# Kernel tuning notes

Hardware: AMD Instinct MI355X
Metric: run time of the kernel (lower is better)

## Reference

```python
import jax, jax.numpy as jnp
import numpy as np

LE_LAMBDA = 0.01  # le_lambda from __init__
V, D = 100000, 128
B, C, NEG, P = 16384, 10, 50, 2000


def setup_inputs() -> dict:
    key = jax.random.key(0)
    k1, k2, k3, k4, k5, k6 = jax.random.split(key, 6)
    return {
        "input_labels": jax.random.randint(k1, (B,), 0, V),
        "pos_labels": jax.random.randint(k2, (B, C), 0, V),
        "neg_labels": jax.random.randint(k3, (B, NEG), 0, V),
        "pairs": jax.random.randint(k4, (P, 2), 0, V),
        "in_embed": jax.random.normal(k5, (V, D), dtype=jnp.float32),
        "out_embed": jax.random.normal(k6, (V, D), dtype=jnp.float32),
    }


def reference(input_labels, pos_labels, neg_labels, pairs, in_embed, out_embed):
    # --- skip-gram negative-sampling loss ---
    ie = in_embed[input_labels]          # [B, D]
    pe = out_embed[pos_labels]           # [B, C, D]
    ne = out_embed[neg_labels]           # [B, NEG, D]
    pos_dot = jnp.einsum('bcd,bd->bc', pe, ie)    # bmm(pos, input.unsqueeze(2))
    neg_dot = jnp.einsum('bkd,bd->bk', ne, -ie)   # bmm(neg, -input)
    log_pos = jax.nn.log_sigmoid(pos_dot).sum(axis=1)
    log_neg = jax.nn.log_sigmoid(neg_dot).sum(axis=1)
    loss_graph = (-(log_pos + log_neg)).mean()
    # --- hierarchy L2 regularizer (vectorized over the pair loop) ---
    diff = in_embed[pairs[:, 0]] - in_embed[pairs[:, 1]]   # [P, D]
    l2_norm = jnp.sqrt((diff * diff).sum(axis=-1)).sum()   # sum of per-pair norms
    loss_le = 0.5 * (l2_norm ** 2) * LE_LAMBDA
    loss_combined = loss_graph + loss_le
    return (loss_combined, loss_le)
```

## Files before the change

kernel.cpp:

```cpp
#include <hip/hip_runtime.h>

#define VOCAB 100000
#define DIM   128
#define BATCH 16384
#define CPOS  10
#define NNEG  50
#define NPAIR 2000
#define LE_LAMBDA 0.01

#define NTOT (CPOS + NNEG)
#define PAIR_BLOCKS ((NPAIR + 7) / 8)

__device__ __forceinline__ float fast_log_sigmoid(float x) {
    float e = __expf(-fabsf(x));
    return fminf(x, 0.0f) - __logf(1.0f + e);
}


__global__ __launch_bounds__(256) void fused_kernel(
    const int* __restrict__ input_labels,
    const int* __restrict__ pos_labels,
    const int* __restrict__ neg_labels,
    const int* __restrict__ pairs,
    const float* __restrict__ in_embed,
    const float* __restrict__ out_embed,
    float* __restrict__ ws)
{
    const int tid    = threadIdx.x;
    const int lane32 = tid & 31;
    const int half   = tid >> 5;

    if (blockIdx.x < BATCH) {
        const int b  = blockIdx.x;
        const int il = input_labels[b];
        const float4 ie = *reinterpret_cast<const float4*>(
            in_embed + (size_t)il * DIM + lane32 * 4);

        int lbl[8];
        #pragma unroll
        for (int k = 0; k < 8; ++k) {
            int j = half + 8 * k;
            if (j < NTOT)
                lbl[k] = (j < CPOS) ? pos_labels[b * CPOS + j]
                                    : neg_labels[b * NNEG + (j - CPOS)];
        }

        float acc = 0.0f;
        #pragma unroll
        for (int k0 = 0; k0 < 8; k0 += 4) {
            float4 oe[4];
            #pragma unroll
            for (int u = 0; u < 4; ++u) {
                int j = half + 8 * (k0 + u);
                if (j < NTOT)
                    oe[u] = *reinterpret_cast<const float4*>(
                        out_embed + (size_t)lbl[k0 + u] * DIM + lane32 * 4);
            }
            #pragma unroll
            for (int u = 0; u < 4; ++u) {
                int j = half + 8 * (k0 + u);
                if (j < NTOT) {
                    float p = ie.x * oe[u].x + ie.y * oe[u].y
                            + ie.z * oe[u].z + ie.w * oe[u].w;
                    p += __shfl_xor(p, 1);
                    p += __shfl_xor(p, 2);
                    p += __shfl_xor(p, 4);
                    p += __shfl_xor(p, 8);
                    p += __shfl_xor(p, 16);
                    acc += fast_log_sigmoid(j < CPOS ? p : -p);
                }
            }
        }

        __shared__ float sred[8];
        if (lane32 == 0) sred[half] = acc;
        __syncthreads();
        if (tid == 0) {
            float s = 0.0f;
            #pragma unroll
            for (int h = 0; h < 8; ++h) s += sred[h];
            ws[b] = s;
        }
    } else {
        const int pb = blockIdx.x - BATCH;
        const int p  = pb * 8 + half;
        if (p < NPAIR) {
            const int a = pairs[p * 2 + 0];
            const int c = pairs[p * 2 + 1];
            const float4 ea = *reinterpret_cast<const float4*>(
                in_embed + (size_t)a * DIM + lane32 * 4);
            const float4 eb = *reinterpret_cast<const float4*>(
                in_embed + (size_t)c * DIM + lane32 * 4);
            const float dx = ea.x - eb.x, dy = ea.y - eb.y;
            const float dz = ea.z - eb.z, dw = ea.w - eb.w;
            float ss = dx * dx + dy * dy + dz * dz + dw * dw;
            ss += __shfl_xor(ss, 1);
            ss += __shfl_xor(ss, 2);
            ss += __shfl_xor(ss, 4);
            ss += __shfl_xor(ss, 8);
            ss += __shfl_xor(ss, 16);
            if (lane32 == 0) ws[BATCH + p] = sqrtf(ss);
        }
    }
}

__global__ __launch_bounds__(256) void finalize_kernel(
    const float* __restrict__ ws, float* __restrict__ out)
{
    const int tid  = threadIdx.x;
    const int lane = tid & 63;
    const int wid  = tid >> 6;

    double g = 0.0, pn = 0.0;
    for (int i = tid; i < BATCH; i += 256) g  += (double)ws[i];
    for (int i = tid; i < NPAIR; i += 256) pn += (double)ws[BATCH + i];

    #pragma unroll
    for (int m = 32; m > 0; m >>= 1) {
        g  += __shfl_xor(g,  m);
        pn += __shfl_xor(pn, m);
    }

    __shared__ double sg[4], sp[4];
    if (lane == 0) { sg[wid] = g; sp[wid] = pn; }
    __syncthreads();
    if (tid == 0) {
        double G = 0.0, PN = 0.0;
        #pragma unroll
        for (int w = 0; w < 4; ++w) { G += sg[w]; PN += sp[w]; }
        const double loss_graph = -G / (double)BATCH;
        const double loss_le    = 0.5 * PN * PN * LE_LAMBDA;
        out[0] = (float)(loss_graph + loss_le);
        out[1] = (float)loss_le;
    }
}

extern "C" void kernel_launch(void* const* d_in, const int* in_sizes, int n_in,
                              void* d_out, int out_size, void* d_ws, size_t ws_size,
                              hipStream_t stream) {
    const int*   input_labels = (const int*)  d_in[0];
    const int*   pos_labels   = (const int*)  d_in[1];
    const int*   neg_labels   = (const int*)  d_in[2];
    const int*   pairs        = (const int*)  d_in[3];
    const float* in_embed     = (const float*)d_in[4];
    const float* out_embed    = (const float*)d_in[5];
    float* out = (float*)d_out;
    float* ws  = (float*)d_ws;

    fused_kernel<<<BATCH + PAIR_BLOCKS, 256, 0, stream>>>(
        input_labels, pos_labels, neg_labels, pairs, in_embed, out_embed, ws);
    finalize_kernel<<<1, 256, 0, stream>>>(ws, out);
}
```

Measured before the change: 194.1 us.

## Map one batch row per wavefront with shuffle-broadcast labels, drop block sync

Each 64-lane wavefront now handles one batch row, so a 256-thread block covers four rows instead of one. The 60 labels are loaded once, one per lane, and broadcast with __shfl, where before each half-wave loaded its own. Each 32-lane half processes 30 targets in unrolled groups of six gathers. The final reduction is a single cross-half shuffle instead of shared memory plus __syncthreads. This cuts the block count, the redundant label loads and the block-level synchronisation, at the cost of more per-thread registers for the six in-flight float4 gathers.

```diff
diff --git a/kernel.cpp b/kernel.cpp
--- a/kernel.cpp
+++ b/kernel.cpp
@@ -9,6 +9,7 @@
 #define LE_LAMBDA 0.01
 
 #define NTOT (CPOS + NNEG)
+#define SGNS_BLOCKS (BATCH / 4)
 #define PAIR_BLOCKS ((NPAIR + 7) / 8)
 
 __device__ __forceinline__ float fast_log_sigmoid(float x) {
@@ -27,63 +28,57 @@
     float* __restrict__ ws)
 {
     const int tid    = threadIdx.x;
+    const int lane64 = tid & 63;
     const int lane32 = tid & 31;
-    const int half   = tid >> 5;
 
-    if (blockIdx.x < BATCH) {
-        const int b  = blockIdx.x;
+    if (blockIdx.x < SGNS_BLOCKS) {
+        const int wid = tid >> 6;
+        const int b   = blockIdx.x * 4 + wid;
+        const int h   = (tid >> 5) & 1;
+
         const int il = input_labels[b];
         const float4 ie = *reinterpret_cast<const float4*>(
             in_embed + (size_t)il * DIM + lane32 * 4);
 
-        int lbl[8];
+        int lblv = 0;
+        if (lane64 < CPOS)       lblv = pos_labels[b * CPOS + lane64];
+        else if (lane64 < NTOT)  lblv = neg_labels[b * NNEG + (lane64 - CPOS)];
+
+        const int jbase = h * 30;
+        float acc = 0.0f;
+
         #pragma unroll
-        for (int k = 0; k < 8; ++k) {
-            int j = half + 8 * k;
-            if (j < NTOT)
-                lbl[k] = (j < CPOS) ? pos_labels[b * CPOS + j]
-                                    : neg_labels[b * NNEG + (j - CPOS)];
-        }
+        for (int k0 = 0; k0 < 30; k0 += 6) {
+            int idx[6];
+            #pragma unroll
+            for (int u = 0; u < 6; ++u)
+                idx[u] = __shfl(lblv, jbase + k0 + u, 64);
 
-        float acc = 0.0f;
-        #pragma unroll
-        for (int k0 = 0; k0 < 8; k0 += 4) {
-            float4 oe[4];
+            float4 oe[6];
             #pragma unroll
-            for (int u = 0; u < 4; ++u) {
-                int j = half + 8 * (k0 + u);
-                if (j < NTOT)
-                    oe[u] = *reinterpret_cast<const float4*>(
-                        out_embed + (size_t)lbl[k0 + u] * DIM + lane32 * 4);
-            }
+            for (int u = 0; u < 6; ++u)
+                oe[u] = *reinterpret_cast<const float4*>(
+                    out_embed + (size_t)idx[u] * DIM + lane32 * 4);
+
             #pragma unroll
-            for (int u = 0; u < 4; ++u) {
-                int j = half + 8 * (k0 + u);
-                if (j < NTOT) {
-                    float p = ie.x * oe[u].x + ie.y * oe[u].y
-                            + ie.z * oe[u].z + ie.w * oe[u].w;
-                    p += __shfl_xor(p, 1);
-                    p += __shfl_xor(p, 2);
-                    p += __shfl_xor(p, 4);
-                    p += __shfl_xor(p, 8);
-                    p += __shfl_xor(p, 16);
-                    acc += fast_log_sigmoid(j < CPOS ? p : -p);
-                }
+            for (int u = 0; u < 6; ++u) {
+                const int j = jbase + k0 + u;
+                float p = ie.x * oe[u].x + ie.y * oe[u].y
+                        + ie.z * oe[u].z + ie.w * oe[u].w;
+                p += __shfl_xor(p, 1);
+                p += __shfl_xor(p, 2);
+                p += __shfl_xor(p, 4);
+                p += __shfl_xor(p, 8);
+                p += __shfl_xor(p, 16);
+                acc += fast_log_sigmoid(j < CPOS ? p : -p);
             }
         }
 
-        __shared__ float sred[8];
-        if (lane32 == 0) sred[half] = acc;
-        __syncthreads();
-        if (tid == 0) {
-            float s = 0.0f;
-            #pragma unroll
-            for (int h = 0; h < 8; ++h) s += sred[h];
-            ws[b] = s;
-        }
+        acc += __shfl_xor(acc, 32);
+        if (lane64 == 0) ws[b] = acc;
     } else {
-        const int pb = blockIdx.x - BATCH;
-        const int p  = pb * 8 + half;
+        const int pb = blockIdx.x - SGNS_BLOCKS;
+        const int p  = pb * 8 + (tid >> 5);
         if (p < NPAIR) {
             const int a = pairs[p * 2 + 0];
             const int c = pairs[p * 2 + 1];
@@ -147,7 +142,7 @@
     float* out = (float*)d_out;
     float* ws  = (float*)d_ws;
 
-    fused_kernel<<<BATCH + PAIR_BLOCKS, 256, 0, stream>>>(
+    fused_kernel<<<SGNS_BLOCKS + PAIR_BLOCKS, 256, 0, stream>>>(
         input_labels, pos_labels, neg_labels, pairs, in_embed, out_embed, ws);
     finalize_kernel<<<1, 256, 0, stream>>>(ws, out);
 }
```

Result: no change. 192.3 us (-0.9%).
